# Optimization experiments

Hardware: AMD Instinct MI355X
Metric: run time of the kernel (lower is better)

## Reference

```python
import jax, jax.numpy as jnp
import numpy as np

B, N_CTX, N_AGENT = 32, 512, 64
D, T, TIME_EMB, HEADS, MLP_H, D_MODEL = 256, 80, 64, 8, 128, 4
HEAD_DIM = D // HEADS


def setup_inputs() -> dict:
    key = jax.random.key(0)
    ks = jax.random.split(key, 12)
    rn = lambda k, s: jax.random.normal(k, s, dtype=jnp.float32) * 0.02
    return {
        'context_feat': jax.random.normal(ks[0], (B, N_CTX, D), dtype=jnp.float32),
        'agent_feat': jax.random.normal(ks[1], (B, N_AGENT, D), dtype=jnp.float32),
        'time_emb': rn(ks[2], (T, TIME_EMB)),
        'time_proj_w': rn(ks[3], (D, TIME_EMB)),
        'time_proj_b': jnp.zeros((D,), jnp.float32),
        'in_proj_w': rn(ks[4], (3 * D, D)),
        'in_proj_b': jnp.zeros((3 * D,), jnp.float32),
        'out_proj_w': rn(ks[5], (D, D)),
        'out_proj_b': jnp.zeros((D,), jnp.float32),
        'mlp_w1': rn(ks[6], (MLP_H, 2 * D)),
        'mlp_b1': jnp.zeros((MLP_H,), jnp.float32),
        'mlp_w2': rn(ks[7], (MLP_H, MLP_H)),
        'mlp_b2': jnp.zeros((MLP_H,), jnp.float32),
        'mlp_w3': rn(ks[8], (1, MLP_H)),
        'mlp_b3': jnp.zeros((1,), jnp.float32),
        'maskemb_w': rn(ks[9], (D_MODEL, 1)),
        'maskemb_b': jnp.zeros((D_MODEL,), jnp.float32),
        'emb_scale': jnp.array(1.0, dtype=jnp.float32),
    }


def reference(context_feat, agent_feat, time_emb, time_proj_w, time_proj_b,
              in_proj_w, in_proj_b, out_proj_w, out_proj_b,
              mlp_w1, mlp_b1, mlp_w2, mlp_b2, mlp_w3, mlp_b3,
              maskemb_w, maskemb_b, emb_scale):
    Bq, N_ctx, _ = context_feat.shape
    N_agent = agent_feat.shape[1]
    Tq = time_emb.shape[0]

    # Time-query: embedding table -> linear proj (Q is identical across batch)
    q_in = time_emb @ time_proj_w.T + time_proj_b                       # [T, D]

    # torch nn.MultiheadAttention: packed in_proj, scale = 1/sqrt(head_dim)
    wq, wk, wv = jnp.split(in_proj_w, 3, axis=0)
    bq, bk, bv = jnp.split(in_proj_b, 3)
    q = (q_in @ wq.T + bq).reshape(Tq, HEADS, HEAD_DIM)                 # [T, H, hd]
    k = (context_feat @ wk.T + bk).reshape(Bq, N_ctx, HEADS, HEAD_DIM)  # [B, S, H, hd]
    v = (context_feat @ wv.T + bv).reshape(Bq, N_ctx, HEADS, HEAD_DIM)

    scale = 1.0 / jnp.sqrt(jnp.asarray(HEAD_DIM, dtype=q.dtype))
    scores = jnp.einsum('thd,bshd->bhts', q * scale, k)                 # [B, H, T, S]
    attn = jax.nn.softmax(scores, axis=-1)
    attn_out = jnp.einsum('bhts,bshd->bthd', attn, v).reshape(Bq, Tq, D)
    attn_out = attn_out @ out_proj_w.T + out_proj_b                     # [B, T, D]

    # MLP on concat([agent_expanded, attn_expanded]) == split first linear
    # into agent half + attn half; never materialize the [B,N,T,2D] tensor.
    w1_agent, w1_attn = mlp_w1[:, :D], mlp_w1[:, D:]
    agent_part = agent_feat @ w1_agent.T                                # [B, N, MLP_H]
    attn_part = attn_out @ w1_attn.T                                    # [B, T, MLP_H]
    h = jax.nn.silu(agent_part[:, :, None, :] + attn_part[:, None, :, :] + mlp_b1)
    h = jax.nn.silu(h @ mlp_w2.T + mlp_b2)                              # [B, N, T, MLP_H]
    logits = (h @ mlp_w3.T + mlp_b3)[..., 0]                            # [B, N, T]

    mask = jax.nn.sigmoid(logits)
    mask_emb = (mask[..., None] @ maskemb_w.T + maskemb_b) * emb_scale  # [B, N, T, d_model]
    return mask, mask_emb
```

## Files before the change

### kernel.cpp

```cpp
#include <hip/hip_runtime.h>
#include <hip/hip_bf16.h>
#include <math.h>

#define BB 32
#define NCTX 512
#define NAG 64
#define DD 256
#define TT 80
#define TEMB 64
#define NH 8
#define HD 32
#define MH 128


typedef __attribute__((ext_vector_type(8))) short short8;
typedef __attribute__((ext_vector_type(4))) float f32x4;
typedef __attribute__((ext_vector_type(4))) unsigned short us4;

static __device__ inline ushort f2b(float f) {
  __hip_bfloat16 h = __float2bfloat16(f);
  return *reinterpret_cast<const ushort*>(&h);
}
static __device__ inline float b2f(ushort u) {
  __hip_bfloat16 h = *reinterpret_cast<const __hip_bfloat16*>(&u);
  return __bfloat162float(h);
}
static __device__ inline us4 pack4(float a, float b, float c, float d) {
  us4 r = {f2b(a), f2b(b), f2b(c), f2b(d)};
  return r;
}
static __device__ inline float rcpf(float x) { return __builtin_amdgcn_rcpf(x); }

#define OPART 655360
#define LPART 20480

__global__ __launch_bounds__(256) void k_P(
    const float* __restrict__ temb, const float* __restrict__ tw,
    const float* __restrict__ tb, const float* __restrict__ inw,
    const float* __restrict__ inb, const float* __restrict__ w1,
    const float* __restrict__ outw, const float* __restrict__ outb,
    const float* __restrict__ agent, const float* __restrict__ context,
    float* __restrict__ q, ushort* __restrict__ wfb, float* __restrict__ bf,
    ushort* __restrict__ agentpb,
    ushort* __restrict__ kb, ushort* __restrict__ vb) {
  __shared__ __align__(16) char sm[51456];
  const int blk = blockIdx.x;
  const int tid = threadIdx.x;
  const int w = tid >> 6, lane = tid & 63;
  const int lgrp = lane >> 4, lcol = lane & 15;
  const int kgrp = lgrp << 3;
  f32x4 zero = {0.f, 0.f, 0.f, 0.f};

  if (blk < 4) {
    ushort (*Tb)[72]  = (ushort(*)[72])sm;
    ushort (*Twb)[72] = (ushort(*)[72])(sm + 11520);
    ushort (*Qs)[264] = (ushort(*)[264])sm;
    ushort (*Bq)[72]  = (ushort(*)[72])(sm + 42240);
    #pragma unroll
    for (int l = 0; l < 5; ++l) {
      int e4 = tid + 256 * l;
      int t = e4 >> 4, k4 = (e4 & 15) << 2;
      float4 v = *(const float4*)&temb[t * TEMB + k4];
      *(us4*)&Tb[t][k4] = pack4(v.x, v.y, v.z, v.w);
    }
    #pragma unroll
    for (int l = 0; l < 16; ++l) {
      int e4 = tid + 256 * l;
      int r = e4 >> 4, k4 = (e4 & 15) << 2;
      float4 v = *(const float4*)&tw[r * TEMB + k4];
      *(us4*)&Twb[r][k4] = pack4(v.x, v.y, v.z, v.w);
    }
    __syncthreads();
    f32x4 acc1[5][4];
    #pragma unroll
    for (int mt = 0; mt < 5; ++mt)
      #pragma unroll
      for (int nt = 0; nt < 4; ++nt) acc1[mt][nt] = zero;
    #pragma unroll
    for (int ks = 0; ks < 2; ++ks) {
      #pragma unroll
      for (int mt = 0; mt < 5; ++mt) {
        short8 af = *(const short8*)&Tb[(mt << 4) + lcol][(ks << 5) + kgrp];
        #pragma unroll
        for (int nt = 0; nt < 4; ++nt) {
          short8 bfr = *(const short8*)&Twb[(w << 6) + (nt << 4) + lcol][(ks << 5) + kgrp];
          acc1[mt][nt] = __builtin_amdgcn_mfma_f32_16x16x32_bf16(af, bfr, acc1[mt][nt], 0, 0, 0);
        }
      }
    }
    __syncthreads();
    #pragma unroll
    for (int mt = 0; mt < 5; ++mt)
      #pragma unroll
      for (int nt = 0; nt < 4; ++nt) {
        int n = (w << 6) + (nt << 4) + lcol;
        float tbn = tb[n];
        #pragma unroll
        for (int r = 0; r < 4; ++r)
          Qs[(mt << 4) + (lgrp << 2) + r][n] = f2b(acc1[mt][nt][r] + tbn);
      }
    __syncthreads();
    const int n0q = blk << 6;
    f32x4 acc2[5] = {zero, zero, zero, zero, zero};
    for (int kc = 0; kc < 4; ++kc) {
      #pragma unroll
      for (int l = 0; l < 4; ++l) {
        int e4 = tid + 256 * l;
        int n = e4 >> 4, k4 = (e4 & 15) << 2;
        float4 v = *(const float4*)&inw[(size_t)(n0q + n) * DD + (kc << 6) + k4];
        *(us4*)&Bq[n][k4] = pack4(v.x, v.y, v.z, v.w);
      }
      __syncthreads();
      #pragma unroll
      for (int ks = 0; ks < 2; ++ks) {
        short8 bfr = *(const short8*)&Bq[(w << 4) + lcol][(ks << 5) + kgrp];
        #pragma unroll
        for (int mt = 0; mt < 5; ++mt) {
          short8 af = *(const short8*)&Qs[(mt << 4) + lcol][(kc << 6) + (ks << 5) + kgrp];
          acc2[mt] = __builtin_amdgcn_mfma_f32_16x16x32_bf16(af, bfr, acc2[mt], 0, 0, 0);
        }
      }
      __syncthreads();
    }
    int n = n0q + (w << 4) + lcol;
    float bn = inb[n];
    #pragma unroll
    for (int mt = 0; mt < 5; ++mt)
      #pragma unroll
      for (int r = 0; r < 4; ++r) {
        int m = (mt << 4) + (lgrp << 2) + r;
        q[m * DD + n] = (acc2[mt][r] + bn) * 0.17677669529663687f;
      }
  } else if (blk < 132) {
    int i = blk - 4, j = tid;
    float* w1row = (float*)sm;
    float* red   = (float*)(sm + 1024);
    w1row[j] = w1[i * 2 * DD + DD + j];
    __syncthreads();
    float acc = 0.f;
    for (int k = 0; k < DD; ++k) acc += w1row[k] * outw[k * DD + j];
    wfb[i * DD + j] = f2b(acc);
    red[j] = w1row[j] * outb[j];
    __syncthreads();
    for (int s2 = 128; s2 > 0; s2 >>= 1) {
      if (j < s2) red[j] += red[j + s2];
      __syncthreads();
    }
    if (j == 0) bf[i] = red[0];
  } else if (blk < 196) {
    int gb = blk - 132;
    const int m0 = (gb >> 1) << 6;
    const int n0 = (gb & 1) << 6;
    ushort (*Ab)[72] = (ushort(*)[72])sm;
    ushort (*Bb)[72] = (ushort(*)[72])(sm + 9216);
    f32x4 acc[4] = {zero, zero, zero, zero};
    for (int k0 = 0; k0 < 256; k0 += 64) {
      __syncthreads();
      #pragma unroll
      for (int l = 0; l < 4; ++l) {
        int e = tid + 256 * l;
        int m = e >> 4, k4 = (e & 15) << 2;
        float4 va = *(const float4*)&agent[(size_t)(m0 + m) * 256 + k0 + k4];
        *(us4*)&Ab[m][k4] = pack4(va.x, va.y, va.z, va.w);
        float4 vb2 = *(const float4*)&w1[(size_t)(n0 + m) * 512 + k0 + k4];
        *(us4*)&Bb[m][k4] = pack4(vb2.x, vb2.y, vb2.z, vb2.w);
      }
      __syncthreads();
      #pragma unroll
      for (int kk = 0; kk < 64; kk += 32) {
        short8 af = *(const short8*)&Ab[(w << 4) + lcol][kk + kgrp];
        #pragma unroll
        for (int tc = 0; tc < 4; ++tc) {
          short8 bfr = *(const short8*)&Bb[(tc << 4) + lcol][kk + kgrp];
          acc[tc] = __builtin_amdgcn_mfma_f32_16x16x32_bf16(af, bfr, acc[tc], 0, 0, 0);
        }
      }
    }
    #pragma unroll
    for (int tc = 0; tc < 4; ++tc) {
      int n = n0 + (tc << 4) + lcol;
      #pragma unroll
      for (int r = 0; r < 4; ++r) {
        int m = m0 + (w << 4) + (lgrp << 2) + r;
        agentpb[(size_t)m * MH + n] = f2b(acc[tc][r]);
      }
    }
  } else {
    int kb2 = blk - 196;
    const int m0 = (kb2 & 255) << 6;
    const int n0 = (kb2 >> 8) << 7;
    ushort (*Ab)[72] = (ushort(*)[72])sm;
    ushort (*Bb)[72] = (ushort(*)[72])(sm + 9216);
    const float* Wm = inw + 256 * 256;
    const float* bkv = inb + 256;
    f32x4 acc[8];
    #pragma unroll
    for (int tc = 0; tc < 8; ++tc) acc[tc] = zero;
    for (int k0 = 0; k0 < 256; k0 += 64) {
      __syncthreads();
      #pragma unroll
      for (int l = 0; l < 4; ++l) {
        int e = tid + 256 * l;
        int m = e >> 4, k4 = (e & 15) << 2;
        float4 v = *(const float4*)&context[(size_t)(m0 + m) * 256 + k0 + k4];
        *(us4*)&Ab[m][k4] = pack4(v.x, v.y, v.z, v.w);
      }
      #pragma unroll
      for (int l = 0; l < 8; ++l) {
        int e = tid + 256 * l;
        int n = e >> 4, k4 = (e & 15) << 2;
        float4 v = *(const float4*)&Wm[(size_t)(n0 + n) * 256 + k0 + k4];
        *(us4*)&Bb[n][k4] = pack4(v.x, v.y, v.z, v.w);
      }
      __syncthreads();
      #pragma unroll
      for (int kk = 0; kk < 64; kk += 32) {
        short8 af = *(const short8*)&Ab[(w << 4) + lcol][kk + kgrp];
        #pragma unroll
        for (int tc = 0; tc < 8; ++tc) {
          short8 bfr = *(const short8*)&Bb[(tc << 4) + lcol][kk + kgrp];
          acc[tc] = __builtin_amdgcn_mfma_f32_16x16x32_bf16(af, bfr, acc[tc], 0, 0, 0);
        }
      }
    }
    #pragma unroll
    for (int tc = 0; tc < 8; ++tc) {
      int n = n0 + (tc << 4) + lcol;
      float bias = bkv[n];
      int h = (n >> 5) & 7, hd = n & 31;
      #pragma unroll
      for (int r = 0; r < 4; ++r) {
        int m = m0 + (w << 4) + (lgrp << 2) + r;
        int bl = m >> 9, s = m & 511;
        ushort v = f2b(acc[tc][r] + bias);
        if (n < 256)
          kb[(((size_t)(bl * NH + h)) * NCTX + s) * HD + hd] = v;
        else
          vb[(((size_t)(bl * NH + h)) * HD + hd) * NCTX + s] = v;
      }
    }
  }
}

__global__ __launch_bounds__(256) void k_B(
    const float* __restrict__ q, const ushort* __restrict__ kg,
    const ushort* __restrict__ vtg, float* __restrict__ oP,
    float* __restrict__ lP) {
  __shared__ __align__(16) char sm[47104];
  ushort (*Qb)[40]  = (ushort(*)[40])(sm);
  ushort (*Kb)[40]  = (ushort(*)[40])(sm + 6400);
  ushort (*Vb)[136] = (ushort(*)[136])(sm + 16640);
  ushort (*Pb)[136] = (ushort(*)[136])(sm + 25344);
  float  (*Ored)[80][32] = (float(*)[80][32])(sm);
  float  (*lred)[80] = (float(*)[80])(sm + 40960);
  const int blk = blockIdx.x;
  const int bhl = blk >> 1, part = blk & 1;
  const int h = bhl & 7;
  const int tid = threadIdx.x;
  const int w = tid >> 6, lane = tid & 63;
  const int lgrp = lane >> 4, lcol = lane & 15;
  const int kgrp = lgrp << 3;
  const ushort* kp = kg + (size_t)bhl * NCTX * HD;
  const ushort* vp = vtg + (size_t)bhl * HD * NCTX;
  #pragma unroll
  for (int l = 0; l < 3; ++l) {
    int e4 = tid + 256 * l;
    if (e4 < 640) {
      int t = e4 >> 3, d4 = (e4 & 7) << 2;
      float4 v = *(const float4*)&q[t * DD + h * HD + d4];
      *(us4*)&Qb[t][d4] = pack4(v.x, v.y, v.z, v.w);
    }
  }
  f32x4 zero = {0.f, 0.f, 0.f, 0.f};
  f32x4 oacc[5][2];
  #pragma unroll
  for (int tt = 0; tt < 5; ++tt) { oacc[tt][0] = zero; oacc[tt][1] = zero; }
  float lpart[5] = {0.f, 0.f, 0.f, 0.f, 0.f};
  for (int c = 0; c < 2; ++c) {
    const int s0 = part * 256 + c * 128;
    __syncthreads();
    #pragma unroll
    for (int l = 0; l < 2; ++l) {
      int e = tid + 256 * l;
      int sl = e >> 2, d8 = (e & 3) << 3;
      *(short8*)&Kb[sl][d8] = *(const short8*)&kp[(size_t)(s0 + sl) * HD + d8];
      int d = e >> 4, s8 = (e & 15) << 3;
      *(short8*)&Vb[d][s8] = *(const short8*)&vp[(size_t)d * NCTX + s0 + s8];
    }
    __syncthreads();
    f32x4 sacc[2][5];
    #pragma unroll
    for (int st = 0; st < 2; ++st) {
      short8 af = *(const short8*)&Kb[(w << 5) + (st << 4) + lcol][kgrp];
      #pragma unroll
      for (int tt = 0; tt < 5; ++tt) {
        short8 bfr = *(const short8*)&Qb[(tt << 4) + lcol][kgrp];
        sacc[st][tt] = __builtin_amdgcn_mfma_f32_16x16x32_bf16(af, bfr, zero, 0, 0, 0);
      }
    }
    #pragma unroll
    for (int st = 0; st < 2; ++st) {
      #pragma unroll
      for (int tt = 0; tt < 5; ++tt) {
        float p0 = __expf(sacc[st][tt][0]), p1 = __expf(sacc[st][tt][1]);
        float p2 = __expf(sacc[st][tt][2]), p3 = __expf(sacc[st][tt][3]);
        ushort u0 = f2b(p0), u1 = f2b(p1), u2 = f2b(p2), u3 = f2b(p3);
        lpart[tt] += b2f(u0) + b2f(u1) + b2f(u2) + b2f(u3);
        uint2 pk;
        pk.x = (uint)u0 | ((uint)u1 << 16);
        pk.y = (uint)u2 | ((uint)u3 << 16);
        *(uint2*)&Pb[(tt << 4) + lcol][(w << 5) + (st << 4) + (lgrp << 2)] = pk;
      }
    }
    __syncthreads();
    #pragma unroll
    for (int tt = 0; tt < 5; ++tt) {
      short8 pa = *(const short8*)&Pb[(tt << 4) + lcol][(w << 5) + kgrp];
      #pragma unroll
      for (int dt = 0; dt < 2; ++dt) {
        short8 vbr = *(const short8*)&Vb[(dt << 4) + lcol][(w << 5) + kgrp];
        oacc[tt][dt] = __builtin_amdgcn_mfma_f32_16x16x32_bf16(pa, vbr, oacc[tt][dt], 0, 0, 0);
      }
    }
  }
  __syncthreads();
  #pragma unroll
  for (int tt = 0; tt < 5; ++tt) {
    float l = lpart[tt];
    l += __shfl_xor(l, 16); l += __shfl_xor(l, 32);
    if (lane < 16) lred[w][(tt << 4) + lane] = l;
    #pragma unroll
    for (int dt = 0; dt < 2; ++dt)
      #pragma unroll
      for (int r = 0; r < 4; ++r)
        Ored[w][(tt << 4) + (lgrp << 2) + r][(dt << 4) + lcol] = oacc[tt][dt][r];
  }
  __syncthreads();
  float* op = oP + (size_t)part * OPART + (size_t)bhl * TT * HD;
  for (int i = tid; i < TT * HD; i += 256) {
    int t = i >> 5, d = i & 31;
    op[i] = Ored[0][t][d] + Ored[1][t][d] + Ored[2][t][d] + Ored[3][t][d];
  }
  for (int t = tid; t < TT; t += 256)
    lP[(size_t)part * LPART + (size_t)bhl * TT + t] =
        lred[0][t] + lred[1][t] + lred[2][t] + lred[3][t];
}

__global__ __launch_bounds__(256) void k_C(
    const float* __restrict__ oP, const float* __restrict__ lP,
    const ushort* __restrict__ wfb, const float* __restrict__ bfv,
    ushort* __restrict__ attnpb) {
  __shared__ __align__(16) ushort Ab[64][72];
  const int gb = blockIdx.x;
  const int m0 = (gb >> 1) << 6;
  const int n0 = (gb & 1) << 6;
  const int tid = threadIdx.x;
  const int w = tid >> 6, lane = tid & 63;
  const int lgrp = lane >> 4, lcol = lane & 15;
  const int kgrp = lgrp << 3;
  f32x4 zero = {0.f, 0.f, 0.f, 0.f};
  f32x4 acc[4] = {zero, zero, zero, zero};
  for (int k0 = 0; k0 < 256; k0 += 64) {
    __syncthreads();
    #pragma unroll
    for (int l = 0; l < 4; ++l) {
      int e = tid + 256 * l;
      int m = e >> 4, c4 = (e & 15) << 2;
      int row = m0 + m;
      int bg = row / 80, t = row - bg * 80;
      int dfull = k0 + c4, h = dfull >> 5, hd = dfull & 31;
      size_t bh = (size_t)(bg * NH + h);
      const float* o0 = &oP[(bh * TT + t) * HD + hd];
      float4 a0 = *(const float4*)o0;
      float4 a1 = *(const float4*)(o0 + OPART);
      float li = rcpf(lP[bh * TT + t] + lP[LPART + bh * TT + t]);
      *(us4*)&Ab[m][c4] = pack4((a0.x + a1.x) * li, (a0.y + a1.y) * li,
                                (a0.z + a1.z) * li, (a0.w + a1.w) * li);
    }
    __syncthreads();
    #pragma unroll
    for (int kk = 0; kk < 64; kk += 32) {
      short8 af = *(const short8*)&Ab[(w << 4) + lcol][kk + kgrp];
      #pragma unroll
      for (int tc = 0; tc < 4; ++tc) {
        short8 bfr = *(const short8*)&wfb[(size_t)(n0 + (tc << 4) + lcol) * 256 + k0 + kk + kgrp];
        acc[tc] = __builtin_amdgcn_mfma_f32_16x16x32_bf16(af, bfr, acc[tc], 0, 0, 0);
      }
    }
  }
  #pragma unroll
  for (int tc = 0; tc < 4; ++tc) {
    int n = n0 + (tc << 4) + lcol;
    float bv = bfv[n];
    #pragma unroll
    for (int r = 0; r < 4; ++r) {
      int m = m0 + (w << 4) + (lgrp << 2) + r;
      attnpb[(size_t)m * MH + n] = f2b(acc[tc][r] + bv);
    }
  }
}

__global__ __launch_bounds__(256) void k_D(
    const ushort* __restrict__ agentpb, const ushort* __restrict__ attnpb,
    const float* __restrict__ w2, const float* __restrict__ b1g,
    const float* __restrict__ b2g, const float* __restrict__ w3,
    const float* __restrict__ b3, const float* __restrict__ mew,
    const float* __restrict__ meb, const float* __restrict__ esc,
    float* __restrict__ mask_out, float* __restrict__ emb_out) {
  const int a0 = blockIdx.y * 8;
  const int b = blockIdx.z;
  const int tid = threadIdx.x;
  __shared__ ushort Xb[64][136];
  __shared__ ushort Wb[128][136];
  #pragma unroll
  for (int l = 0; l < 16; ++l) {
    int e4 = tid + 256 * l;
    int o = e4 >> 5, k4 = (e4 & 31) << 2;
    float4 v = *(const float4*)&w2[(size_t)o * MH + k4];
    *(us4*)&Wb[o][k4] = pack4(v.x, v.y, v.z, v.w);
  }
  const int w = tid >> 6, lane = tid & 63;
  const int lgrp = lane >> 4, lcol = lane & 15;
  const int kgrp = lgrp << 3;
  f32x4 zero = {0.f, 0.f, 0.f, 0.f};
  float es = esc[0], b3v = b3[0];
  float m0 = mew[0], m1 = mew[1], m2 = mew[2], m3 = mew[3];
  float e0 = meb[0], e1 = meb[1], e2 = meb[2], e3 = meb[3];
  for (int rep = 0; rep < 2; ++rep) {
    const int t0 = blockIdx.x * 16 + rep * 8;
    __syncthreads();
    #pragma unroll
    for (int l = 0; l < 8; ++l) {
      int e4 = tid + 256 * l;
      int tok = e4 >> 5, k4 = (e4 & 31) << 2;
      int a = a0 + (tok >> 3), t = t0 + (tok & 7);
      us4 au = *(const us4*)&agentpb[((size_t)b * NAG + a) * MH + k4];
      us4 tu = *(const us4*)&attnpb[((size_t)b * TT + t) * MH + k4];
      float4 bb = *(const float4*)&b1g[k4];
      float x0 = b2f(au[0]) + b2f(tu[0]) + bb.x;
      float x1 = b2f(au[1]) + b2f(tu[1]) + bb.y;
      float x2 = b2f(au[2]) + b2f(tu[2]) + bb.z;
      float x3 = b2f(au[3]) + b2f(tu[3]) + bb.w;
      *(us4*)&Xb[tok][k4] = pack4(x0 * rcpf(1.f + __expf(-x0)),
                                  x1 * rcpf(1.f + __expf(-x1)),
                                  x2 * rcpf(1.f + __expf(-x2)),
                                  x3 * rcpf(1.f + __expf(-x3)));
    }
    __syncthreads();
    f32x4 acc[8] = {zero, zero, zero, zero, zero, zero, zero, zero};
    #pragma unroll
    for (int k0 = 0; k0 < MH; k0 += 32) {
      short8 af = *(const short8*)&Xb[(w << 4) + lcol][k0 + kgrp];
      #pragma unroll
      for (int tc = 0; tc < 8; ++tc) {
        short8 bfr = *(const short8*)&Wb[(tc << 4) + lcol][k0 + kgrp];
        acc[tc] = __builtin_amdgcn_mfma_f32_16x16x32_bf16(af, bfr, acc[tc], 0, 0, 0);
      }
    }
    float psum[4] = {0.f, 0.f, 0.f, 0.f};
    #pragma unroll
    for (int tc = 0; tc < 8; ++tc) {
      int o = (tc << 4) + lcol;
      float b2o = b2g[o], w3o = w3[o];
      #pragma unroll
      for (int r = 0; r < 4; ++r) {
        float hv = acc[tc][r] + b2o;
        hv = hv * rcpf(1.f + __expf(-hv));
        psum[r] += hv * w3o;
      }
    }
    #pragma unroll
    for (int r = 0; r < 4; ++r) {
      float p = psum[r];
      p += __shfl_xor(p, 1); p += __shfl_xor(p, 2);
      p += __shfl_xor(p, 4); p += __shfl_xor(p, 8);
      if (lcol == 0) {
        int tok = (w << 4) + (lgrp << 2) + r;
        int a = a0 + (tok >> 3), t = t0 + (tok & 7);
        float mask = rcpf(1.f + __expf(-(p + b3v)));
        size_t mi = ((size_t)b * NAG + a) * TT + t;
        mask_out[mi] = mask;
        emb_out[mi * 4 + 0] = (mask * m0 + e0) * es;
        emb_out[mi * 4 + 1] = (mask * m1 + e1) * es;
        emb_out[mi * 4 + 2] = (mask * m2 + e2) * es;
        emb_out[mi * 4 + 3] = (mask * m3 + e3) * es;
      }
    }
  }
}

extern "C" void kernel_launch(void* const* d_in, const int* in_sizes, int n_in,
                              void* d_out, int out_size, void* d_ws, size_t ws_size,
                              hipStream_t stream) {
  const float* context = (const float*)d_in[0];
  const float* agent   = (const float*)d_in[1];
  const float* temb    = (const float*)d_in[2];
  const float* tw      = (const float*)d_in[3];
  const float* tb      = (const float*)d_in[4];
  const float* inw     = (const float*)d_in[5];
  const float* inb     = (const float*)d_in[6];
  const float* outw    = (const float*)d_in[7];
  const float* outb    = (const float*)d_in[8];
  const float* w1      = (const float*)d_in[9];
  const float* b1      = (const float*)d_in[10];
  const float* w2      = (const float*)d_in[11];
  const float* b2      = (const float*)d_in[12];
  const float* w3      = (const float*)d_in[13];
  const float* b3      = (const float*)d_in[14];
  const float* mew     = (const float*)d_in[15];
  const float* meb     = (const float*)d_in[16];
  const float* esc     = (const float*)d_in[17];

  float* ws = (float*)d_ws;
  float* q   = ws + 0;
  float* bf  = ws + 20480;
  float* oP  = ws + 20608;
  float* lP  = ws + 1331328;
  ushort* u16 = (ushort*)(ws + 1372288);
  ushort* wfb     = u16;
  ushort* agentpb = u16 + 32768;
  ushort* attnpb  = u16 + 294912;
  ushort* kbufb   = u16 + 622592;
  ushort* vbufb   = u16 + 4816896;

  float* mask_out = (float*)d_out;
  float* emb_out  = mask_out + (size_t)BB * NAG * TT;

  k_P<<<dim3(196 + 1024), dim3(256), 0, stream>>>(
      temb, tw, tb, inw, inb, w1, outw, outb, agent, context,
      q, wfb, bf, agentpb, kbufb, vbufb);
  k_B<<<dim3(512), dim3(256), 0, stream>>>(
      q, kbufb, vbufb, oP, lP);
  k_C<<<dim3(80), dim3(256), 0, stream>>>(oP, lP, wfb, bf, attnpb);
  k_D<<<dim3(5, 8, 32), dim3(256), 0, stream>>>(
      agentpb, attnpb, w2, b1, b2, w3, b3, mew, meb, esc, mask_out, emb_out);
}
```

Before: 79.15 us.

## Split attention over four context chunks and shrink k_P shared memory

The attention kernel now splits the 512-long context into four 128-wide chunks per (batch, head) instead of two, launching 1024 blocks with no inner loop. The combine kernel sums four partial outputs and four normaliser partials. Separately, the time-query projection in k_P stages its intermediate through a global bf16 buffer and processes it in windows, cutting the kernel's static LDS footprint so more blocks can be resident per CU. The tradeoff is extra partial-buffer traffic and workspace, plus global round-trips for the small q path.

```diff
diff --git a/kernel.cpp b/kernel.cpp
--- a/kernel.cpp
+++ b/kernel.cpp
@@ -40,10 +40,11 @@
     const float* __restrict__ inb, const float* __restrict__ w1,
     const float* __restrict__ outw, const float* __restrict__ outb,
     const float* __restrict__ agent, const float* __restrict__ context,
-    float* __restrict__ q, ushort* __restrict__ wfb, float* __restrict__ bf,
+    float* __restrict__ q, ushort* __restrict__ q_inb,
+    ushort* __restrict__ wfb, float* __restrict__ bf,
     ushort* __restrict__ agentpb,
     ushort* __restrict__ kb, ushort* __restrict__ vb) {
-  __shared__ __align__(16) char sm[51456];
+  __shared__ __align__(16) char sm[30976];
   const int blk = blockIdx.x;
   const int tid = threadIdx.x;
   const int w = tid >> 6, lane = tid & 63;
@@ -52,10 +53,10 @@
   f32x4 zero = {0.f, 0.f, 0.f, 0.f};
 
   if (blk < 4) {
-    ushort (*Tb)[72]  = (ushort(*)[72])sm;
-    ushort (*Twb)[72] = (ushort(*)[72])(sm + 11520);
-    ushort (*Qs)[264] = (ushort(*)[264])sm;
-    ushort (*Bq)[72]  = (ushort(*)[72])(sm + 42240);
+    ushort (*Tb)[72]   = (ushort(*)[72])sm;
+    ushort (*Twin)[72] = (ushort(*)[72])(sm + 11520);
+    ushort (*Qs)[136]  = (ushort(*)[136])sm;
+    ushort (*Bq)[72]   = (ushort(*)[72])(sm + 21760);
     #pragma unroll
     for (int l = 0; l < 5; ++l) {
       int e4 = tid + 256 * l;
@@ -63,64 +64,65 @@
       float4 v = *(const float4*)&temb[t * TEMB + k4];
       *(us4*)&Tb[t][k4] = pack4(v.x, v.y, v.z, v.w);
     }
-    #pragma unroll
-    for (int l = 0; l < 16; ++l) {
-      int e4 = tid + 256 * l;
-      int r = e4 >> 4, k4 = (e4 & 15) << 2;
-      float4 v = *(const float4*)&tw[r * TEMB + k4];
-      *(us4*)&Twb[r][k4] = pack4(v.x, v.y, v.z, v.w);
-    }
-    __syncthreads();
-    f32x4 acc1[5][4];
-    #pragma unroll
-    for (int mt = 0; mt < 5; ++mt)
-      #pragma unroll
-      for (int nt = 0; nt < 4; ++nt) acc1[mt][nt] = zero;
-    #pragma unroll
-    for (int ks = 0; ks < 2; ++ks) {
-      #pragma unroll
-      for (int mt = 0; mt < 5; ++mt) {
-        short8 af = *(const short8*)&Tb[(mt << 4) + lcol][(ks << 5) + kgrp];
+    for (int win = 0; win < 4; ++win) {
+      __syncthreads();
+      #pragma unroll
+      for (int l = 0; l < 4; ++l) {
+        int e4 = tid + 256 * l;
+        int r = e4 >> 4, k4 = (e4 & 15) << 2;
+        float4 v = *(const float4*)&tw[(size_t)((win << 6) + r) * TEMB + k4];
+        *(us4*)&Twin[r][k4] = pack4(v.x, v.y, v.z, v.w);
+      }
+      __syncthreads();
+      f32x4 accw[5] = {zero, zero, zero, zero, zero};
+      #pragma unroll
+      for (int ks = 0; ks < 2; ++ks) {
+        short8 bfr = *(const short8*)&Twin[(w << 4) + lcol][(ks << 5) + kgrp];
         #pragma unroll
-        for (int nt = 0; nt < 4; ++nt) {
-          short8 bfr = *(const short8*)&Twb[(w << 6) + (nt << 4) + lcol][(ks << 5) + kgrp];
-          acc1[mt][nt] = __builtin_amdgcn_mfma_f32_16x16x32_bf16(af, bfr, acc1[mt][nt], 0, 0, 0);
+        for (int mt = 0; mt < 5; ++mt) {
+          short8 af = *(const short8*)&Tb[(mt << 4) + lcol][(ks << 5) + kgrp];
+          accw[mt] = __builtin_amdgcn_mfma_f32_16x16x32_bf16(af, bfr, accw[mt], 0, 0, 0);
         }
       }
-    }
-    __syncthreads();
-    #pragma unroll
-    for (int mt = 0; mt < 5; ++mt)
-      #pragma unroll
-      for (int nt = 0; nt < 4; ++nt) {
-        int n = (w << 6) + (nt << 4) + lcol;
-        float tbn = tb[n];
+      int n = (win << 6) + (w << 4) + lcol;
+      float tbn = tb[n];
+      #pragma unroll
+      for (int mt = 0; mt < 5; ++mt)
         #pragma unroll
         for (int r = 0; r < 4; ++r)
-          Qs[(mt << 4) + (lgrp << 2) + r][n] = f2b(acc1[mt][nt][r] + tbn);
-      }
-    __syncthreads();
+          q_inb[(size_t)((mt << 4) + (lgrp << 2) + r) * DD + n] =
+              f2b(accw[mt][r] + tbn);
+    }
     const int n0q = blk << 6;
     f32x4 acc2[5] = {zero, zero, zero, zero, zero};
-    for (int kc = 0; kc < 4; ++kc) {
-      #pragma unroll
-      for (int l = 0; l < 4; ++l) {
+    for (int half = 0; half < 2; ++half) {
+      __syncthreads();
+      #pragma unroll
+      for (int l = 0; l < 10; ++l) {
         int e4 = tid + 256 * l;
-        int n = e4 >> 4, k4 = (e4 & 15) << 2;
-        float4 v = *(const float4*)&inw[(size_t)(n0q + n) * DD + (kc << 6) + k4];
-        *(us4*)&Bq[n][k4] = pack4(v.x, v.y, v.z, v.w);
-      }
-      __syncthreads();
-      #pragma unroll
-      for (int ks = 0; ks < 2; ++ks) {
-        short8 bfr = *(const short8*)&Bq[(w << 4) + lcol][(ks << 5) + kgrp];
+        int t = e4 >> 5, k4 = (e4 & 31) << 2;
+        *(us4*)&Qs[t][k4] = *(const us4*)&q_inb[(size_t)t * DD + (half << 7) + k4];
+      }
+      for (int kc = 0; kc < 2; ++kc) {
+        __syncthreads();
         #pragma unroll
-        for (int mt = 0; mt < 5; ++mt) {
-          short8 af = *(const short8*)&Qs[(mt << 4) + lcol][(kc << 6) + (ks << 5) + kgrp];
-          acc2[mt] = __builtin_amdgcn_mfma_f32_16x16x32_bf16(af, bfr, acc2[mt], 0, 0, 0);
+        for (int l = 0; l < 4; ++l) {
+          int e4 = tid + 256 * l;
+          int n = e4 >> 4, k4 = (e4 & 15) << 2;
+          float4 v = *(const float4*)&inw[(size_t)(n0q + n) * DD + (half << 7) + (kc << 6) + k4];
+          *(us4*)&Bq[n][k4] = pack4(v.x, v.y, v.z, v.w);
         }
-      }
-      __syncthreads();
+        __syncthreads();
+        #pragma unroll
+        for (int ks = 0; ks < 2; ++ks) {
+          short8 bfr = *(const short8*)&Bq[(w << 4) + lcol][(ks << 5) + kgrp];
+          #pragma unroll
+          for (int mt = 0; mt < 5; ++mt) {
+            short8 af = *(const short8*)&Qs[(mt << 4) + lcol][(kc << 6) + (ks << 5) + kgrp];
+            acc2[mt] = __builtin_amdgcn_mfma_f32_16x16x32_bf16(af, bfr, acc2[mt], 0, 0, 0);
+          }
+        }
+      }
     }
     int n = n0q + (w << 4) + lcol;
     float bn = inb[n];
@@ -254,8 +256,9 @@
   float  (*Ored)[80][32] = (float(*)[80][32])(sm);
   float  (*lred)[80] = (float(*)[80])(sm + 40960);
   const int blk = blockIdx.x;
-  const int bhl = blk >> 1, part = blk & 1;
+  const int bhl = blk >> 2, part = blk & 3;
   const int h = bhl & 7;
+  const int s0 = part << 7;
   const int tid = threadIdx.x;
   const int w = tid >> 6, lane = tid & 63;
   const int lgrp = lane >> 4, lcol = lane & 15;
@@ -271,56 +274,52 @@
       *(us4*)&Qb[t][d4] = pack4(v.x, v.y, v.z, v.w);
     }
   }
+  #pragma unroll
+  for (int l = 0; l < 2; ++l) {
+    int e = tid + 256 * l;
+    int sl = e >> 2, d8 = (e & 3) << 3;
+    *(short8*)&Kb[sl][d8] = *(const short8*)&kp[(size_t)(s0 + sl) * HD + d8];
+    int d = e >> 4, s8 = (e & 15) << 3;
+    *(short8*)&Vb[d][s8] = *(const short8*)&vp[(size_t)d * NCTX + s0 + s8];
+  }
+  __syncthreads();
   f32x4 zero = {0.f, 0.f, 0.f, 0.f};
   f32x4 oacc[5][2];
   #pragma unroll
   for (int tt = 0; tt < 5; ++tt) { oacc[tt][0] = zero; oacc[tt][1] = zero; }
   float lpart[5] = {0.f, 0.f, 0.f, 0.f, 0.f};
-  for (int c = 0; c < 2; ++c) {
-    const int s0 = part * 256 + c * 128;
-    __syncthreads();
-    #pragma unroll
-    for (int l = 0; l < 2; ++l) {
-      int e = tid + 256 * l;
-      int sl = e >> 2, d8 = (e & 3) << 3;
-      *(short8*)&Kb[sl][d8] = *(const short8*)&kp[(size_t)(s0 + sl) * HD + d8];
-      int d = e >> 4, s8 = (e & 15) << 3;
-      *(short8*)&Vb[d][s8] = *(const short8*)&vp[(size_t)d * NCTX + s0 + s8];
-    }
-    __syncthreads();
-    f32x4 sacc[2][5];
-    #pragma unroll
-    for (int st = 0; st < 2; ++st) {
-      short8 af = *(const short8*)&Kb[(w << 5) + (st << 4) + lcol][kgrp];
-      #pragma unroll
-      for (int tt = 0; tt < 5; ++tt) {
-        short8 bfr = *(const short8*)&Qb[(tt << 4) + lcol][kgrp];
-        sacc[st][tt] = __builtin_amdgcn_mfma_f32_16x16x32_bf16(af, bfr, zero, 0, 0, 0);
-      }
-    }
-    #pragma unroll
-    for (int st = 0; st < 2; ++st) {
-      #pragma unroll
-      for (int tt = 0; tt < 5; ++tt) {
-        float p0 = __expf(sacc[st][tt][0]), p1 = __expf(sacc[st][tt][1]);
-        float p2 = __expf(sacc[st][tt][2]), p3 = __expf(sacc[st][tt][3]);
-        ushort u0 = f2b(p0), u1 = f2b(p1), u2 = f2b(p2), u3 = f2b(p3);
-        lpart[tt] += b2f(u0) + b2f(u1) + b2f(u2) + b2f(u3);
-        uint2 pk;
-        pk.x = (uint)u0 | ((uint)u1 << 16);
-        pk.y = (uint)u2 | ((uint)u3 << 16);
-        *(uint2*)&Pb[(tt << 4) + lcol][(w << 5) + (st << 4) + (lgrp << 2)] = pk;
-      }
-    }
-    __syncthreads();
+  f32x4 sacc[2][5];
+  #pragma unroll
+  for (int st = 0; st < 2; ++st) {
+    short8 af = *(const short8*)&Kb[(w << 5) + (st << 4) + lcol][kgrp];
     #pragma unroll
     for (int tt = 0; tt < 5; ++tt) {
-      short8 pa = *(const short8*)&Pb[(tt << 4) + lcol][(w << 5) + kgrp];
-      #pragma unroll
-      for (int dt = 0; dt < 2; ++dt) {
-        short8 vbr = *(const short8*)&Vb[(dt << 4) + lcol][(w << 5) + kgrp];
-        oacc[tt][dt] = __builtin_amdgcn_mfma_f32_16x16x32_bf16(pa, vbr, oacc[tt][dt], 0, 0, 0);
-      }
+      short8 bfr = *(const short8*)&Qb[(tt << 4) + lcol][kgrp];
+      sacc[st][tt] = __builtin_amdgcn_mfma_f32_16x16x32_bf16(af, bfr, zero, 0, 0, 0);
+    }
+  }
+  #pragma unroll
+  for (int st = 0; st < 2; ++st) {
+    #pragma unroll
+    for (int tt = 0; tt < 5; ++tt) {
+      float p0 = __expf(sacc[st][tt][0]), p1 = __expf(sacc[st][tt][1]);
+      float p2 = __expf(sacc[st][tt][2]), p3 = __expf(sacc[st][tt][3]);
+      ushort u0 = f2b(p0), u1 = f2b(p1), u2 = f2b(p2), u3 = f2b(p3);
+      lpart[tt] += b2f(u0) + b2f(u1) + b2f(u2) + b2f(u3);
+      uint2 pk;
+      pk.x = (uint)u0 | ((uint)u1 << 16);
+      pk.y = (uint)u2 | ((uint)u3 << 16);
+      *(uint2*)&Pb[(tt << 4) + lcol][(w << 5) + (st << 4) + (lgrp << 2)] = pk;
+    }
+  }
+  __syncthreads();
+  #pragma unroll
+  for (int tt = 0; tt < 5; ++tt) {
+    short8 pa = *(const short8*)&Pb[(tt << 4) + lcol][(w << 5) + kgrp];
+    #pragma unroll
+    for (int dt = 0; dt < 2; ++dt) {
+      short8 vbr = *(const short8*)&Vb[(dt << 4) + lcol][(w << 5) + kgrp];
+      oacc[tt][dt] = __builtin_amdgcn_mfma_f32_16x16x32_bf16(pa, vbr, oacc[tt][dt], 0, 0, 0);
     }
   }
   __syncthreads();
@@ -373,9 +372,15 @@
       const float* o0 = &oP[(bh * TT + t) * HD + hd];
       float4 a0 = *(const float4*)o0;
       float4 a1 = *(const float4*)(o0 + OPART);
-      float li = rcpf(lP[bh * TT + t] + lP[LPART + bh * TT + t]);
-      *(us4*)&Ab[m][c4] = pack4((a0.x + a1.x) * li, (a0.y + a1.y) * li,
-                                (a0.z + a1.z) * li, (a0.w + a1.w) * li);
+      float4 a2 = *(const float4*)(o0 + 2 * OPART);
+      float4 a3 = *(const float4*)(o0 + 3 * OPART);
+      size_t lidx = bh * TT + t;
+      float li = rcpf(lP[lidx] + lP[LPART + lidx] +
+                      lP[2 * LPART + lidx] + lP[3 * LPART + lidx]);
+      *(us4*)&Ab[m][c4] = pack4((a0.x + a1.x + a2.x + a3.x) * li,
+                                (a0.y + a1.y + a2.y + a3.y) * li,
+                                (a0.z + a1.z + a2.z + a3.z) * li,
+                                (a0.w + a1.w + a2.w + a3.w) * li);
     }
     __syncthreads();
     #pragma unroll
@@ -515,21 +520,22 @@
   float* q   = ws + 0;
   float* bf  = ws + 20480;
   float* oP  = ws + 20608;
-  float* lP  = ws + 1331328;
-  ushort* u16 = (ushort*)(ws + 1372288);
+  float* lP  = ws + 2642048;
+  ushort* u16 = (ushort*)(ws + 2723968);
   ushort* wfb     = u16;
   ushort* agentpb = u16 + 32768;
   ushort* attnpb  = u16 + 294912;
   ushort* kbufb   = u16 + 622592;
   ushort* vbufb   = u16 + 4816896;
+  ushort* q_inb   = u16 + 9011200;
 
   float* mask_out = (float*)d_out;
   float* emb_out  = mask_out + (size_t)BB * NAG * TT;
 
   k_P<<<dim3(196 + 1024), dim3(256), 0, stream>>>(
       temb, tw, tb, inw, inb, w1, outw, outb, agent, context,
-      q, wfb, bf, agentpb, kbufb, vbufb);
-  k_B<<<dim3(512), dim3(256), 0, stream>>>(
+      q, q_inb, wfb, bf, agentpb, kbufb, vbufb);
+  k_B<<<dim3(1024), dim3(256), 0, stream>>>(
       q, kbufb, vbufb, oP, lP);
   k_C<<<dim3(80), dim3(256), 0, stream>>>(oP, lP, wfb, bf, attnpb);
   k_D<<<dim3(5, 8, 32), dim3(256), 0, stream>>>(
```

Result: slower. 103.4 us (+30.7%).
